# Kernel optimization log

Hardware: AMD Instinct MI355X
Metric: run time of the kernel (lower is better)

The kernel has to match this reference:

```python
import jax, jax.numpy as jnp
import numpy as np

B, I, J, DIM, H, DH = 2, 2048, 2048, 512, 8, 64
INNER = H * DH  # 512
SCALE = DH ** -0.5


def setup_inputs() -> dict:
    key = jax.random.key(0)
    ks = jax.random.split(key, 10)
    w = lambda k, shp: jax.random.normal(k, shp, dtype=jnp.float32) * 0.02
    return {
        "x": jax.random.normal(ks[0], (B, I, DIM), dtype=jnp.float32),
        "context": jax.random.normal(ks[1], (B, J, DIM), dtype=jnp.float32),
        "w_qk": w(ks[2], (DIM, INNER)),
        "w_cqk": w(ks[3], (DIM, INNER)),
        "w_v": w(ks[4], (DIM, INNER)),
        "w_cv": w(ks[5], (DIM, INNER)),
        "w_out": w(ks[6], (INNER, DIM)),
        "b_out": jnp.zeros((DIM,), dtype=jnp.float32),
        "w_cout": w(ks[7], (INNER, DIM)),
        "b_cout": jnp.zeros((DIM,), dtype=jnp.float32),
    }


def _split_heads(t):
    # [b, n, h*d] -> [b, h, n, d]
    b, n, _ = t.shape
    return t.reshape(b, n, H, DH).transpose(0, 2, 1, 3)


def reference(x, context, w_qk, w_cqk, w_v, w_cv, w_out, b_out, w_cout, b_cout):
    # projections (no bias, matching nn.Linear(..., bias=False))
    qk = _split_heads(x @ w_qk)            # [b,h,i,d]
    cqk = _split_heads(context @ w_cqk)    # [b,h,j,d]
    v = _split_heads(x @ w_v)              # [b,h,i,d]
    cv = _split_heads(context @ w_cv)      # [b,h,j,d]

    sim = jnp.einsum('bhid,bhjd->bhij', qk, cqk) * SCALE  # [b,h,i,j]

    attn = jax.nn.softmax(sim, axis=-1)        # row softmax over j
    context_attn = jax.nn.softmax(sim, axis=-2)  # column softmax over i

    out = jnp.einsum('bhij,bhjd->bhid', attn, cv)           # [b,h,i,d]
    context_out = jnp.einsum('bhji,bhjd->bhid', context_attn, v)  # [b,h,j_out=i? -> per einsum: i indexes last of attn]

    # merge heads: [b,h,n,d] -> [b,n,h*d]
    merge = lambda t: t.transpose(0, 2, 1, 3).reshape(t.shape[0], t.shape[2], INNER)
    out = merge(out) @ w_out + b_out                    # [b,i,dim]
    context_out = merge(context_out) @ w_cout + b_cout  # [b,j,dim]
    return (out, context_out)
```

## Files before the change

kernel.cpp:

```cpp
#include <hip/hip_runtime.h>

#define DEVI __device__ __forceinline__

typedef __attribute__((ext_vector_type(8))) short short8;
typedef __attribute__((ext_vector_type(4))) float f32x4;

struct alignas(8) us4 { unsigned short a, b, c, d; };

DEVI unsigned short f2bf(float f) {
    unsigned int u = __float_as_uint(f);
    u += 0x7fffU + ((u >> 16) & 1U);
    return (unsigned short)(u >> 16);
}

DEVI f32x4 mfma16(short8 a, short8 b, f32x4 c) {
    return __builtin_amdgcn_mfma_f32_16x16x32_bf16(a, b, c, 0, 0, 0);
}

DEVI unsigned pk2(float lo, float hi) {
    unsigned r0 = __float_as_uint(lo) + 0x8000u;
    unsigned r1 = __float_as_uint(hi) + 0x8000u;
    return __builtin_amdgcn_perm(r1, r0, 0x07060302u);
}

DEVI short8 mk8(unsigned a, unsigned b, unsigned c, unsigned d) {
    union { unsigned u[4]; short8 s; } x;
    x.u[0] = a; x.u[1] = b; x.u[2] = c; x.u[3] = d;
    return x.s;
}

#define GLDS(gp, sp) __builtin_amdgcn_global_load_lds( \
    (const __attribute__((address_space(1))) void*)(gp), \
    (__attribute__((address_space(3))) void*)(sp), 16, 0, 0)

#define VMCNT(n) asm volatile("s_waitcnt vmcnt(" #n ")" ::: "memory")

#define SQC 0.42466089f

__global__ __launch_bounds__(256) void prep_kernel(
    const float* __restrict__ x, const float* __restrict__ ctx,
    const float* w0, const float* w1, const float* w2, const float* w3,
    const float* w4, const float* w5,
    short* __restrict__ Xb, short* __restrict__ Cb, short* __restrict__ wT)
{
    int z = blockIdx.z;
    if (z < 2) {
        const float* s = z ? ctx : x;
        short* d = z ? Cb : Xb;
        size_t t = (size_t)blockIdx.x * 256 + threadIdx.x;
        float4 v = *(const float4*)(s + t * 4);
        us4 o = { f2bf(v.x), f2bf(v.y), f2bf(v.z), f2bf(v.w) };
        *(us4*)(d + t * 4) = o;
        return;
    }
    if (blockIdx.x >= 384) return;
    const float* srcs[6] = {w0, w1, w2, w3, w4, w5};
    int wz = blockIdx.x >> 6, rem = blockIdx.x & 63;
    const float* src = srcs[wz];
    short* dst = wT + (size_t)wz * 262144;
    int k0 = (rem >> 3) * 64, n0 = (rem & 7) * 64;
    __shared__ float tile[64][65];
    int t = threadIdx.x;
    int r = t >> 2, c0 = (t & 3) * 16;
#pragma unroll
    for (int ii = 0; ii < 4; ++ii) {
        float4 v = *(const float4*)(src + (size_t)(k0 + r) * 512 + n0 + c0 + ii * 4);
        tile[r][c0 + ii * 4 + 0] = v.x;
        tile[r][c0 + ii * 4 + 1] = v.y;
        tile[r][c0 + ii * 4 + 2] = v.z;
        tile[r][c0 + ii * 4 + 3] = v.w;
    }
    __syncthreads();
#pragma unroll
    for (int ii = 0; ii < 4; ++ii) {
        us4 o;
        o.a = f2bf(tile[c0 + ii * 4 + 0][r]);
        o.b = f2bf(tile[c0 + ii * 4 + 1][r]);
        o.c = f2bf(tile[c0 + ii * 4 + 2][r]);
        o.d = f2bf(tile[c0 + ii * 4 + 3][r]);
        *(us4*)(dst + (size_t)(n0 + r) * 512 + k0 + c0 + ii * 4) = o;
    }
}

__global__ __launch_bounds__(256, 4) void proj_kernel(
    const short* __restrict__ Xb, const short* __restrict__ Cb,
    const short* __restrict__ wT,
    short* __restrict__ QK, short* __restrict__ CQK,
    short* __restrict__ VT, short* __restrict__ CVT)
{
    __shared__ __align__(16) char smem[17664];
    short (*wst)[4096] = (short (*)[4096])smem;
    float (*ctile)[69] = (float (*)[69])smem;

    int p = blockIdx.z;
    const short* src = (p & 1) ? Cb : Xb;
    const short* wm = wT + (size_t)p * 262144;
    int wid = threadIdx.x >> 6, lane = threadIdx.x & 63, il = lane & 15, q = lane >> 4;
    int mb = blockIdx.x * 64, nb = blockIdx.y * 64;
    int srow = lane >> 3, scol8 = ((lane & 7) ^ srow) << 3;
    int key = il & 7;
    const short* wL0 = wm + (size_t)(nb + wid * 16 + srow) * 512 + scol8;
    const short* wL1 = wL0 + 8 * 512;
#define PSTAGE(buf, ck) do { \
    GLDS(wL0 + (ck) * 64, &wst[buf][wid * 1024]); \
    GLDS(wL1 + (ck) * 64, &wst[buf][wid * 1024 + 512]); } while (0)

    PSTAGE(0, 0);
    const short* arow = src + (size_t)(mb + wid * 16 + il) * 512;
    short8 a[16];
#pragma unroll
    for (int j = 0; j < 16; ++j) a[j] = *(const short8*)(arow + j * 32 + (q << 3));

    f32x4 acc[4] = {};
#pragma unroll
    for (int ck = 0; ck < 8; ++ck) {
        int buf = ck & 1;
        if (ck < 7) { PSTAGE(buf ^ 1, ck + 1); VMCNT(2); } else { VMCNT(0); }
        __builtin_amdgcn_s_barrier();
#pragma unroll
        for (int kk = 0; kk < 2; ++kk) {
#pragma unroll
            for (int nj = 0; nj < 4; ++nj) {
                short8 b = *(const short8*)(&wst[buf][(nj * 16 + il) * 64 + ((((kk << 2) + q) ^ key) << 3)]);
                acc[nj] = mfma16(a[ck * 2 + kk], b, acc[nj]);
            }
        }
        asm volatile("" ::: "memory");
        __builtin_amdgcn_s_barrier();
    }
#undef PSTAGE

#pragma unroll
    for (int nj = 0; nj < 4; ++nj)
#pragma unroll
        for (int r = 0; r < 4; ++r)
            ctile[wid * 16 + q * 4 + r][nj * 16 + il] = acc[nj][r];
    __syncthreads();
    int t = threadIdx.x, row = t >> 2, seg = (t & 3) << 4;
    short tmp[16];
    int h = blockIdx.y;
    if (p < 2) {
        short* dst = p ? CQK : QK;
        int i = mb + row, b2 = i >> 11, iL = i & 2047;
#pragma unroll
        for (int e = 0; e < 16; ++e) tmp[e] = (short)f2bf(ctile[row][seg + e] * SQC);
        short* dp = dst + (((size_t)b2 * 8 + h) * 2048 + iL) * 64 + seg;
        *(short8*)dp = *(const short8*)tmp;
        *(short8*)(dp + 8) = *(const short8*)(tmp + 8);
    } else {
        short* dst = (p == 2) ? VT : CVT;
        int d = row;
        int i0 = mb + seg, b2 = i0 >> 11, iL = i0 & 2047;
#pragma unroll
        for (int e = 0; e < 16; ++e) tmp[e] = (short)f2bf(ctile[seg + e][d]);
        short* dp = dst + (((size_t)b2 * 8 + h) * 64 + d) * 2048 + iL;
        *(short8*)dp = *(const short8*)tmp;
        *(short8*)(dp + 8) = *(const short8*)(tmp + 8);
    }
}

__global__ __launch_bounds__(256, 3) void attn_kernel(
    const short* __restrict__ QK, const short* __restrict__ CQK,
    const short* __restrict__ VT, const short* __restrict__ CVT,
    short* __restrict__ OUTx, short* __restrict__ OUTc)
{
    __shared__ __align__(16) short At[8192];
    __shared__ __align__(16) short Bt[2][4096];
    __shared__ __align__(16) short Wt[2][4096];

    int flat = blockIdx.x + (blockIdx.y << 4) + (blockIdx.z << 8);
    int bh = flat & 15;
    int ib = (flat >> 4) & 15;
    int z = flat >> 8;

    const short* Arows = z ? CQK : QK;
    const short* Bcols = z ? QK : CQK;
    const short* WTm   = z ? VT : CVT;
    short* Om          = z ? OUTc : OUTx;

    int b_ = bh >> 3, h = bh & 7;
    int w = threadIdx.x >> 6, lane = threadIdx.x & 63, il = lane & 15, q = lane >> 4;
    const short* Ab = Arows + (size_t)bh * 131072;
    const short* Bb = Bcols + (size_t)bh * 131072;
    const short* Wb = WTm + (size_t)bh * 131072;

    int srow = lane >> 3;
    int scol8 = ((lane & 7) ^ srow) << 3;
    int key = il & 7;

    int p0 = w * 16 + srow, p1 = p0 + 8;
    int j0p = (p0 & 0x23) | ((p0 & 0x0C) << 1) | ((p0 & 0x10) >> 2);
    int j1p = (p1 & 0x23) | ((p1 & 0x0C) << 1) | ((p1 & 0x10) >> 2);
    const short* BbL0 = Bb + j0p * 64 + scol8;
    const short* BbL1 = Bb + j1p * 64 + scol8;
    const short* WbL0 = Wb + (size_t)p0 * 2048 + scol8;
    const short* WbL1 = WbL0 + 8 * 2048;

#define STAGE(buf, jt) do { \
    GLDS(BbL0 + (jt) * 4096, &Bt[buf][w * 1024]); \
    GLDS(BbL1 + (jt) * 4096, &Bt[buf][w * 1024 + 512]); \
    GLDS(WbL0 + (jt) * 64, &Wt[buf][w * 1024]); \
    GLDS(WbL1 + (jt) * 64, &Wt[buf][w * 1024 + 512]); } while (0)

    {
        const short* AbL = Ab + (size_t)(ib * 128 + w * 32 + srow) * 64 + scol8;
        GLDS(AbL, &At[w * 2048]);
        GLDS(AbL + 512, &At[w * 2048 + 512]);
        GLDS(AbL + 1024, &At[w * 2048 + 1024]);
        GLDS(AbL + 1536, &At[w * 2048 + 1536]);
    }
    STAGE(0, 0);
    VMCNT(4);

    short8 aq[2][2];
#pragma unroll
    for (int rg = 0; rg < 2; ++rg) {
        const short* base = &At[(w * 32 + rg * 16 + il) * 64];
        aq[rg][0] = *(const short8*)(base + ((q ^ key) << 3));
        aq[rg][1] = *(const short8*)(base + (((q + 4) ^ key) << 3));
    }

    f32x4 acc[2][4] = {};
    float s_acc[2] = {0.f, 0.f};

    for (int jt = 0; jt < 32; ++jt) {
        int cur = jt & 1;
        if (jt < 31) { STAGE(cur ^ 1, jt + 1); VMCNT(4); } else { VMCNT(0); }
        __builtin_amdgcn_s_barrier();

        short8 b0[4], b1[4];
#pragma unroll
        for (int nj = 0; nj < 4; ++nj) {
            const short* bb = &Bt[cur][(nj * 16 + il) * 64];
            b0[nj] = *(const short8*)(bb + ((q ^ key) << 3));
            b1[nj] = *(const short8*)(bb + (((q + 4) ^ key) << 3));
        }

        unsigned pw[2][8];
#pragma unroll
        for (int rg = 0; rg < 2; ++rg) {
#pragma unroll
            for (int nj = 0; nj < 4; ++nj) {
                f32x4 zz = {};
                zz = mfma16(b0[nj], aq[rg][0], zz);
                zz = mfma16(b1[nj], aq[rg][1], zz);
                float e0 = __builtin_amdgcn_exp2f(zz[0]);
                float e1 = __builtin_amdgcn_exp2f(zz[1]);
                float e2 = __builtin_amdgcn_exp2f(zz[2]);
                float e3 = __builtin_amdgcn_exp2f(zz[3]);
                s_acc[rg] += (e0 + e1) + (e2 + e3);
                pw[rg][nj * 2 + 0] = pk2(e0, e1);
                pw[rg][nj * 2 + 1] = pk2(e2, e3);
            }
        }
        short8 pa0[2] = { mk8(pw[0][0], pw[0][1], pw[0][2], pw[0][3]),
                          mk8(pw[1][0], pw[1][1], pw[1][2], pw[1][3]) };
        short8 pa1[2] = { mk8(pw[0][4], pw[0][5], pw[0][6], pw[0][7]),
                          mk8(pw[1][4], pw[1][5], pw[1][6], pw[1][7]) };

#pragma unroll
        for (int nd = 0; nd < 4; ++nd) {
            const short* vv = &Wt[cur][(nd * 16 + il) * 64];
            short8 v0 = *(const short8*)(vv + ((q ^ key) << 3));
            short8 v1 = *(const short8*)(vv + (((q + 4) ^ key) << 3));
#pragma unroll
            for (int rg = 0; rg < 2; ++rg) {
                acc[rg][nd] = mfma16(pa0[rg], v0, acc[rg][nd]);
                acc[rg][nd] = mfma16(pa1[rg], v1, acc[rg][nd]);
            }
        }
        asm volatile("" ::: "memory");
        __builtin_amdgcn_s_barrier();
    }
#undef STAGE

    f32x4 inv[2];
#pragma unroll
    for (int rg = 0; rg < 2; ++rg) {
        float s = s_acc[rg];
        s += __shfl_xor(s, 16);
        s += __shfl_xor(s, 32);
#pragma unroll
        for (int r = 0; r < 4; ++r)
            inv[rg][r] = 1.0f / __shfl(s, q * 4 + r);
    }

#pragma unroll
    for (int rg = 0; rg < 2; ++rg) {
#pragma unroll
        for (int nd = 0; nd < 4; ++nd) {
#pragma unroll
            for (int r = 0; r < 4; ++r) {
                int i = ib * 128 + w * 32 + rg * 16 + q * 4 + r;
                Om[((size_t)b_ * 2048 + i) * 512 + h * 64 + nd * 16 + il] =
                    (short)f2bf(acc[rg][nd][r] * inv[rg][r]);
            }
        }
    }
}

__global__ __launch_bounds__(256, 4) void final_kernel(
    const short* __restrict__ OUTx, const short* __restrict__ OUTc,
    const short* __restrict__ wT,
    const float* __restrict__ b_out, const float* __restrict__ b_cout,
    float* __restrict__ dout)
{
    __shared__ __align__(16) short wst[2][4096];
    int z = blockIdx.z;
    const short* Am = z ? OUTc : OUTx;
    const short* wm = wT + (size_t)(4 + z) * 262144;
    const float* bias = z ? b_cout : b_out;
    float* D = dout + (size_t)z * 2097152;
    int wid = threadIdx.x >> 6, lane = threadIdx.x & 63, il = lane & 15, q = lane >> 4;
    int mb = blockIdx.x * 64, nb = blockIdx.y * 64;
    int srow = lane >> 3, scol8 = ((lane & 7) ^ srow) << 3;
    int key = il & 7;
    const short* wL0 = wm + (size_t)(nb + wid * 16 + srow) * 512 + scol8;
    const short* wL1 = wL0 + 8 * 512;
#define FSTAGE(buf, ck) do { \
    GLDS(wL0 + (ck) * 64, &wst[buf][wid * 1024]); \
    GLDS(wL1 + (ck) * 64, &wst[buf][wid * 1024 + 512]); } while (0)

    FSTAGE(0, 0);
    const short* arow = Am + (size_t)(mb + wid * 16 + il) * 512;
    short8 a[16];
#pragma unroll
    for (int j = 0; j < 16; ++j) a[j] = *(const short8*)(arow + j * 32 + (q << 3));

    f32x4 acc[4] = {};
#pragma unroll
    for (int ck = 0; ck < 8; ++ck) {
        int buf = ck & 1;
        if (ck < 7) { FSTAGE(buf ^ 1, ck + 1); VMCNT(2); } else { VMCNT(0); }
        __builtin_amdgcn_s_barrier();
#pragma unroll
        for (int kk = 0; kk < 2; ++kk) {
#pragma unroll
            for (int nj = 0; nj < 4; ++nj) {
                short8 b = *(const short8*)(&wst[buf][(nj * 16 + il) * 64 + ((((kk << 2) + q) ^ key) << 3)]);
                acc[nj] = mfma16(a[ck * 2 + kk], b, acc[nj]);
            }
        }
        asm volatile("" ::: "memory");
        __builtin_amdgcn_s_barrier();
    }
#undef FSTAGE

#pragma unroll
    for (int nj = 0; nj < 4; ++nj) {
        int c = nb + nj * 16 + il;
        float bi = bias[c];
#pragma unroll
        for (int r = 0; r < 4; ++r) {
            int m = mb + wid * 16 + q * 4 + r;
            D[(size_t)m * 512 + c] = acc[nj][r] + bi;
        }
    }
}

extern "C" void kernel_launch(void* const* d_in, const int* in_sizes, int n_in,
                              void* d_out, int out_size, void* d_ws, size_t ws_size,
                              hipStream_t stream)
{
    (void)in_sizes; (void)n_in; (void)out_size; (void)ws_size;
    const float* x      = (const float*)d_in[0];
    const float* ctx    = (const float*)d_in[1];
    const float* w_qk   = (const float*)d_in[2];
    const float* w_cqk  = (const float*)d_in[3];
    const float* w_v    = (const float*)d_in[4];
    const float* w_cv   = (const float*)d_in[5];
    const float* w_out  = (const float*)d_in[6];
    const float* b_out  = (const float*)d_in[7];
    const float* w_cout = (const float*)d_in[8];
    const float* b_cout = (const float*)d_in[9];
    float* dout = (float*)d_out;

    char* ws = (char*)d_ws;
    const size_t WSZ = (size_t)512 * 512 * 2;
    const size_t TSZ = (size_t)16 * 2048 * 64 * 2;
    short* wT   = (short*)ws;
    short* Xb   = (short*)(ws + 6 * WSZ);
    short* Cb   = (short*)(ws + 6 * WSZ + 1 * TSZ);
    short* QK   = (short*)(ws + 6 * WSZ + 2 * TSZ);
    short* CQK  = (short*)(ws + 6 * WSZ + 3 * TSZ);
    short* VT   = (short*)(ws + 6 * WSZ + 4 * TSZ);
    short* CVT  = (short*)(ws + 6 * WSZ + 5 * TSZ);
    short* OUTx = Xb;
    short* OUTc = Cb;

    prep_kernel<<<dim3(2048, 1, 3), 256, 0, stream>>>(
        x, ctx, w_qk, w_cqk, w_v, w_cv, w_out, w_cout, Xb, Cb, wT);
    proj_kernel<<<dim3(64, 8, 4), 256, 0, stream>>>(Xb, Cb, wT, QK, CQK, VT, CVT);
    attn_kernel<<<dim3(16, 16, 2), 256, 0, stream>>>(QK, CQK, VT, CVT, OUTx, OUTc);
    final_kernel<<<dim3(64, 8, 2), 256, 0, stream>>>(OUTx, OUTc, wT, b_out, b_cout, dout);
}
```

Measured before the change: 168.0 us.

## Fuse activation bf16 conversion into projection and use triple-buffered LDS pipelines

```diff
diff --git a/kernel.cpp b/kernel.cpp
--- a/kernel.cpp
+++ b/kernel.cpp
@@ -34,26 +34,15 @@
     (__attribute__((address_space(3))) void*)(sp), 16, 0, 0)
 
 #define VMCNT(n) asm volatile("s_waitcnt vmcnt(" #n ")" ::: "memory")
+#define LGKMCNT0 asm volatile("s_waitcnt lgkmcnt(0)" ::: "memory")
+#define MEMFENCE asm volatile("" ::: "memory")
 
 #define SQC 0.42466089f
 
 __global__ __launch_bounds__(256) void prep_kernel(
-    const float* __restrict__ x, const float* __restrict__ ctx,
     const float* w0, const float* w1, const float* w2, const float* w3,
-    const float* w4, const float* w5,
-    short* __restrict__ Xb, short* __restrict__ Cb, short* __restrict__ wT)
-{
-    int z = blockIdx.z;
-    if (z < 2) {
-        const float* s = z ? ctx : x;
-        short* d = z ? Cb : Xb;
-        size_t t = (size_t)blockIdx.x * 256 + threadIdx.x;
-        float4 v = *(const float4*)(s + t * 4);
-        us4 o = { f2bf(v.x), f2bf(v.y), f2bf(v.z), f2bf(v.w) };
-        *(us4*)(d + t * 4) = o;
-        return;
-    }
-    if (blockIdx.x >= 384) return;
+    const float* w4, const float* w5, short* __restrict__ wT)
+{
     const float* srcs[6] = {w0, w1, w2, w3, w4, w5};
     int wz = blockIdx.x >> 6, rem = blockIdx.x & 63;
     const float* src = srcs[wz];
@@ -83,17 +72,17 @@
 }
 
 __global__ __launch_bounds__(256, 4) void proj_kernel(
-    const short* __restrict__ Xb, const short* __restrict__ Cb,
+    const float* __restrict__ x, const float* __restrict__ ctx,
     const short* __restrict__ wT,
     short* __restrict__ QK, short* __restrict__ CQK,
     short* __restrict__ VT, short* __restrict__ CVT)
 {
-    __shared__ __align__(16) char smem[17664];
+    __shared__ __align__(16) char smem[24576];
     short (*wst)[4096] = (short (*)[4096])smem;
     float (*ctile)[69] = (float (*)[69])smem;
 
     int p = blockIdx.z;
-    const short* src = (p & 1) ? Cb : Xb;
+    const float* src = (p & 1) ? ctx : x;
     const short* wm = wT + (size_t)p * 262144;
     int wid = threadIdx.x >> 6, lane = threadIdx.x & 63, il = lane & 15, q = lane >> 4;
     int mb = blockIdx.x * 64, nb = blockIdx.y * 64;
@@ -101,35 +90,43 @@
     int key = il & 7;
     const short* wL0 = wm + (size_t)(nb + wid * 16 + srow) * 512 + scol8;
     const short* wL1 = wL0 + 8 * 512;
-#define PSTAGE(buf, ck) do { \
-    GLDS(wL0 + (ck) * 64, &wst[buf][wid * 1024]); \
-    GLDS(wL1 + (ck) * 64, &wst[buf][wid * 1024 + 512]); } while (0)
+#define PSTAGE(s, ck) do { \
+    GLDS(wL0 + (ck) * 64, &wst[s][wid * 1024]); \
+    GLDS(wL1 + (ck) * 64, &wst[s][wid * 1024 + 512]); } while (0)
 
     PSTAGE(0, 0);
-    const short* arow = src + (size_t)(mb + wid * 16 + il) * 512;
+    PSTAGE(1, 1);
+
+    const float* arow = src + (size_t)(mb + wid * 16 + il) * 512;
     short8 a[16];
 #pragma unroll
-    for (int j = 0; j < 16; ++j) a[j] = *(const short8*)(arow + j * 32 + (q << 3));
+    for (int j = 0; j < 16; ++j) {
+        float4 f0 = *(const float4*)(arow + j * 32 + q * 8);
+        float4 f1 = *(const float4*)(arow + j * 32 + q * 8 + 4);
+        a[j] = mk8(pk2(f0.x, f0.y), pk2(f0.z, f0.w),
+                   pk2(f1.x, f1.y), pk2(f1.z, f1.w));
+    }
 
     f32x4 acc[4] = {};
-#pragma unroll
+    int sA = 0, sB = 1, sC = 2;
     for (int ck = 0; ck < 8; ++ck) {
-        int buf = ck & 1;
-        if (ck < 7) { PSTAGE(buf ^ 1, ck + 1); VMCNT(2); } else { VMCNT(0); }
+        if (ck < 7) { VMCNT(2); } else { VMCNT(0); }
+        MEMFENCE;
         __builtin_amdgcn_s_barrier();
+        if (ck < 6) PSTAGE(sC, ck + 2);
 #pragma unroll
         for (int kk = 0; kk < 2; ++kk) {
 #pragma unroll
             for (int nj = 0; nj < 4; ++nj) {
-                short8 b = *(const short8*)(&wst[buf][(nj * 16 + il) * 64 + ((((kk << 2) + q) ^ key) << 3)]);
+                short8 b = *(const short8*)(&wst[sA][(nj * 16 + il) * 64 + ((((kk << 2) + q) ^ key) << 3)]);
                 acc[nj] = mfma16(a[ck * 2 + kk], b, acc[nj]);
             }
         }
-        asm volatile("" ::: "memory");
-        __builtin_amdgcn_s_barrier();
+        int t_ = sA; sA = sB; sB = sC; sC = t_;
     }
 #undef PSTAGE
 
+    __syncthreads();
 #pragma unroll
     for (int nj = 0; nj < 4; ++nj)
 #pragma unroll
@@ -164,9 +161,8 @@
     const short* __restrict__ VT, const short* __restrict__ CVT,
     short* __restrict__ OUTx, short* __restrict__ OUTc)
 {
-    __shared__ __align__(16) short At[8192];
-    __shared__ __align__(16) short Bt[2][4096];
-    __shared__ __align__(16) short Wt[2][4096];
+    __shared__ __align__(16) short Bt[3][4096];
+    __shared__ __align__(16) short Wt[3][4096];
 
     int flat = blockIdx.x + (blockIdx.y << 4) + (blockIdx.z << 8);
     int bh = flat & 15;
@@ -196,42 +192,49 @@
     const short* WbL0 = Wb + (size_t)p0 * 2048 + scol8;
     const short* WbL1 = WbL0 + 8 * 2048;
 
-#define STAGE(buf, jt) do { \
-    GLDS(BbL0 + (jt) * 4096, &Bt[buf][w * 1024]); \
-    GLDS(BbL1 + (jt) * 4096, &Bt[buf][w * 1024 + 512]); \
-    GLDS(WbL0 + (jt) * 64, &Wt[buf][w * 1024]); \
-    GLDS(WbL1 + (jt) * 64, &Wt[buf][w * 1024 + 512]); } while (0)
-
+#define STAGE(s, jt) do { \
+    GLDS(BbL0 + (jt) * 4096, &Bt[s][w * 1024]); \
+    GLDS(BbL1 + (jt) * 4096, &Bt[s][w * 1024 + 512]); \
+    GLDS(WbL0 + (jt) * 64, &Wt[s][w * 1024]); \
+    GLDS(WbL1 + (jt) * 64, &Wt[s][w * 1024 + 512]); } while (0)
+
+    short* Areg = (w < 2) ? &Bt[2][0] : &Wt[2][0];
+    int ar = (w & 1) * 2048;
     {
         const short* AbL = Ab + (size_t)(ib * 128 + w * 32 + srow) * 64 + scol8;
-        GLDS(AbL, &At[w * 2048]);
-        GLDS(AbL + 512, &At[w * 2048 + 512]);
-        GLDS(AbL + 1024, &At[w * 2048 + 1024]);
-        GLDS(AbL + 1536, &At[w * 2048 + 1536]);
+        GLDS(AbL, Areg + ar);
+        GLDS(AbL + 512, Areg + ar + 512);
+        GLDS(AbL + 1024, Areg + ar + 1024);
+        GLDS(AbL + 1536, Areg + ar + 1536);
     }
     STAGE(0, 0);
-    VMCNT(4);
+    STAGE(1, 1);
+    VMCNT(8);
 
     short8 aq[2][2];
 #pragma unroll
     for (int rg = 0; rg < 2; ++rg) {
-        const short* base = &At[(w * 32 + rg * 16 + il) * 64];
+        const short* base = Areg + ((w & 1) * 32 + rg * 16 + il) * 64;
         aq[rg][0] = *(const short8*)(base + ((q ^ key) << 3));
         aq[rg][1] = *(const short8*)(base + (((q + 4) ^ key) << 3));
     }
+    LGKMCNT0;
+    __builtin_amdgcn_sched_barrier(0);
 
     f32x4 acc[2][4] = {};
     float s_acc[2] = {0.f, 0.f};
 
+    int sA = 0, sB = 1, sC = 2;
     for (int jt = 0; jt < 32; ++jt) {
-        int cur = jt & 1;
-        if (jt < 31) { STAGE(cur ^ 1, jt + 1); VMCNT(4); } else { VMCNT(0); }
+        if (jt < 31) { VMCNT(4); } else { VMCNT(0); }
+        MEMFENCE;
         __builtin_amdgcn_s_barrier();
+        if (jt < 30) STAGE(sC, jt + 2);
 
         short8 b0[4], b1[4];
 #pragma unroll
         for (int nj = 0; nj < 4; ++nj) {
-            const short* bb = &Bt[cur][(nj * 16 + il) * 64];
+            const short* bb = &Bt[sA][(nj * 16 + il) * 64];
             b0[nj] = *(const short8*)(bb + ((q ^ key) << 3));
             b1[nj] = *(const short8*)(bb + (((q + 4) ^ key) << 3));
         }
@@ -260,7 +263,7 @@
 
 #pragma unroll
         for (int nd = 0; nd < 4; ++nd) {
-            const short* vv = &Wt[cur][(nd * 16 + il) * 64];
+            const short* vv = &Wt[sA][(nd * 16 + il) * 64];
             short8 v0 = *(const short8*)(vv + ((q ^ key) << 3));
             short8 v1 = *(const short8*)(vv + (((q + 4) ^ key) << 3));
 #pragma unroll
@@ -269,8 +272,7 @@
                 acc[rg][nd] = mfma16(pa1[rg], v1, acc[rg][nd]);
             }
         }
-        asm volatile("" ::: "memory");
-        __builtin_amdgcn_s_barrier();
+        int t_ = sA; sA = sB; sB = sC; sC = t_;
     }
 #undef STAGE
 
@@ -305,7 +307,7 @@
     const float* __restrict__ b_out, const float* __restrict__ b_cout,
     float* __restrict__ dout)
 {
-    __shared__ __align__(16) short wst[2][4096];
+    __shared__ __align__(16) short wst[3][4096];
     int z = blockIdx.z;
     const short* Am = z ? OUTc : OUTx;
     const short* wm = wT + (size_t)(4 + z) * 262144;
@@ -317,32 +319,33 @@
     int key = il & 7;
     const short* wL0 = wm + (size_t)(nb + wid * 16 + srow) * 512 + scol8;
     const short* wL1 = wL0 + 8 * 512;
-#define FSTAGE(buf, ck) do { \
-    GLDS(wL0 + (ck) * 64, &wst[buf][wid * 1024]); \
-    GLDS(wL1 + (ck) * 64, &wst[buf][wid * 1024 + 512]); } while (0)
+#define FSTAGE(s, ck) do { \
+    GLDS(wL0 + (ck) * 64, &wst[s][wid * 1024]); \
+    GLDS(wL1 + (ck) * 64, &wst[s][wid * 1024 + 512]); } while (0)
 
     FSTAGE(0, 0);
+    FSTAGE(1, 1);
     const short* arow = Am + (size_t)(mb + wid * 16 + il) * 512;
     short8 a[16];
 #pragma unroll
     for (int j = 0; j < 16; ++j) a[j] = *(const short8*)(arow + j * 32 + (q << 3));
 
     f32x4 acc[4] = {};
-#pragma unroll
+    int sA = 0, sB = 1, sC = 2;
     for (int ck = 0; ck < 8; ++ck) {
-        int buf = ck & 1;
-        if (ck < 7) { FSTAGE(buf ^ 1, ck + 1); VMCNT(2); } else { VMCNT(0); }
+        if (ck < 7) { VMCNT(2); } else { VMCNT(0); }
+        MEMFENCE;
         __builtin_amdgcn_s_barrier();
+        if (ck < 6) FSTAGE(sC, ck + 2);
 #pragma unroll
         for (int kk = 0; kk < 2; ++kk) {
 #pragma unroll
             for (int nj = 0; nj < 4; ++nj) {
-                short8 b = *(const short8*)(&wst[buf][(nj * 16 + il) * 64 + ((((kk << 2) + q) ^ key) << 3)]);
+                short8 b = *(const short8*)(&wst[sA][(nj * 16 + il) * 64 + ((((kk << 2) + q) ^ key) << 3)]);
                 acc[nj] = mfma16(a[ck * 2 + kk], b, acc[nj]);
             }
         }
-        asm volatile("" ::: "memory");
-        __builtin_amdgcn_s_barrier();
+        int t_ = sA; sA = sB; sB = sC; sC = t_;
     }
 #undef FSTAGE
 
@@ -379,18 +382,15 @@
     const size_t WSZ = (size_t)512 * 512 * 2;
     const size_t TSZ = (size_t)16 * 2048 * 64 * 2;
     short* wT   = (short*)ws;
-    short* Xb   = (short*)(ws + 6 * WSZ);
-    short* Cb   = (short*)(ws + 6 * WSZ + 1 * TSZ);
+    short* OUTx = (short*)(ws + 6 * WSZ);
+    short* OUTc = (short*)(ws + 6 * WSZ + 1 * TSZ);
     short* QK   = (short*)(ws + 6 * WSZ + 2 * TSZ);
     short* CQK  = (short*)(ws + 6 * WSZ + 3 * TSZ);
     short* VT   = (short*)(ws + 6 * WSZ + 4 * TSZ);
     short* CVT  = (short*)(ws + 6 * WSZ + 5 * TSZ);
-    short* OUTx = Xb;
-    short* OUTc = Cb;
-
-    prep_kernel<<<dim3(2048, 1, 3), 256, 0, stream>>>(
-        x, ctx, w_qk, w_cqk, w_v, w_cv, w_out, w_cout, Xb, Cb, wT);
-    proj_kernel<<<dim3(64, 8, 4), 256, 0, stream>>>(Xb, Cb, wT, QK, CQK, VT, CVT);
+
+    prep_kernel<<<dim3(384), 256, 0, stream>>>(w_qk, w_cqk, w_v, w_cv, w_out, w_cout, wT);
+    proj_kernel<<<dim3(64, 8, 4), 256, 0, stream>>>(x, ctx, wT, QK, CQK, VT, CVT);
     attn_kernel<<<dim3(16, 16, 2), 256, 0, stream>>>(QK, CQK, VT, CVT, OUTx, OUTc);
     final_kernel<<<dim3(64, 8, 2), 256, 0, stream>>>(OUTx, OUTc, wT, b_out, b_cout, dout);
 }
```

Measured after the change: 176.9 us. 1.05x slower.
